# Performance work log

Measured on AMD Instinct MI355X. Metric: run time of the kernel, lower is better.

## Reference

```python
import jax, jax.numpy as jnp
import numpy as np

H = 2048
I = 8192
E = 8
EI = I // E  # expert_intermediate_size = 1024


def setup_inputs() -> dict:
    key = jax.random.key(0)
    k1, k2, k3 = jax.random.split(key, 3)
    B, N = 4, 4096
    x = jax.random.normal(k1, (B, N, H), dtype=jnp.float32)
    position_ids = jnp.arange(B * N, dtype=jnp.int64).reshape(B, N)
    gate_up_proj = 0.02 * jax.random.normal(k2, (E, H, EI * 2), dtype=jnp.float32)
    down_proj = 0.02 * jax.random.normal(k3, (E, EI, H), dtype=jnp.float32)
    return {"x": x, "position_ids": position_ids,
            "gate_up_proj": gate_up_proj, "down_proj": down_proj}


def reference(x, position_ids, gate_up_proj, down_proj):
    # x: [B,N,H]; position_ids: [B,N] (or [N]); expert = pos % E.
    B, N, Hdim = x.shape
    if position_ids.ndim == 1:
        position_ids = jnp.broadcast_to(position_ids[None, :], (B, N))
    eids = (position_ids % E).reshape(B * N)
    flat = x.reshape(B * N, Hdim)

    # Modulo routing is perfectly balanced (N % E == 0 with sequential ids),
    # so group tokens by expert (stable sort) and run dense per-expert GEMMs
    # instead of per-token gathered-weight bmm (same math, no weight blowup).
    T = B * N
    order = jnp.argsort(eids)          # stable in jax -> tokens grouped by expert
    xg = flat[order].reshape(E, T // E, Hdim)            # [E, T/E, H]
    gu = jnp.einsum('ebh,ehk->ebk', xg, gate_up_proj)    # [E, T/E, 2*EI]
    gate, up = gu[..., :EI], gu[..., EI:]
    inter = jax.nn.silu(gate) * up                       # [E, T/E, EI]
    outg = jnp.einsum('ebi,eih->ebh', inter, down_proj)  # [E, T/E, H]
    out = jnp.zeros((T, Hdim), dtype=x.dtype).at[order].set(outg.reshape(T, Hdim))
    return out.reshape(B, N, Hdim)
```

## Files before the change

kernel.cpp:

```cpp
#include <hip/hip_runtime.h>
#include <hip/hip_bf16.h>

typedef unsigned short u16;
typedef __attribute__((ext_vector_type(8))) short short8;
typedef __attribute__((ext_vector_type(8))) unsigned short u16x8;
typedef __attribute__((ext_vector_type(4))) float f32x4;

#define H_DIM 2048
#define EI_DIM 1024
#define NEXP 8

template <int V> struct IC { static constexpr int value = V; };

__device__ __forceinline__ u16 f2bf(float f) {
  __hip_bfloat16 h = __float2bfloat16(f);
  return __builtin_bit_cast(unsigned short, h);
}

__device__ __forceinline__ void load_lds16(const void* g, void* lds) {
  __builtin_amdgcn_global_load_lds(
      (const __attribute__((address_space(1))) unsigned int*)g,
      (__attribute__((address_space(3))) unsigned int*)lds, 16, 0, 0);
}

__global__ __launch_bounds__(1024) void route_kernel(const int* __restrict__ pid,
                                                     int* __restrict__ offcnt,
                                                     int* __restrict__ order, int T) {
  __shared__ int hist[2048];
  __shared__ int lds[256];
  __shared__ int basel[2048];
  int tid = threadIdx.x, w = tid >> 6, lane = tid & 63;
  unsigned long long below = (1ull << lane) - 1ull;
#pragma unroll 1
  for (int i = 0; i < 16; ++i) {
    int seg = w * 16 + i;
    int eid = pid[seg * 64 + lane] & 7;
#pragma unroll
    for (int e = 0; e < NEXP; ++e) {
      unsigned long long m = __ballot(eid == e);
      if (lane == 0) hist[e * 256 + seg] = __popcll(m);
    }
  }
  __syncthreads();
  int v[8], s = 0;
  if (tid < 256) {
#pragma unroll
    for (int j = 0; j < 8; ++j) { v[j] = hist[tid * 8 + j]; s += v[j]; }
    lds[tid] = s;
  }
  __syncthreads();
  for (int d = 1; d < 256; d <<= 1) {
    int t = (tid < 256 && tid >= d) ? lds[tid - d] : 0;
    __syncthreads();
    if (tid < 256) lds[tid] += t;
    __syncthreads();
  }
  if (tid < 256) {
    int run = lds[tid] - s;
#pragma unroll
    for (int j = 0; j < 8; ++j) { basel[tid * 8 + j] = run; run += v[j]; }
  }
  __syncthreads();
  if (tid < NEXP) {
    int o = basel[tid * 256];
    int nx = (tid < NEXP - 1) ? basel[(tid + 1) * 256] : T;
    offcnt[tid] = o;
    offcnt[8 + tid] = nx - o;
  }
#pragma unroll 1
  for (int i = 0; i < 16; ++i) {
    int seg = w * 16 + i;
    int t = seg * 64 + lane;
    int eid = pid[t] & 7;
#pragma unroll
    for (int e = 0; e < NEXP; ++e) {
      unsigned long long m = __ballot(eid == e);
      if (eid == e) order[basel[e * 256 + seg] + __popcll(m & below)] = t;
    }
  }
}

__device__ __forceinline__ void transpose_tile(const float* __restrict__ in,
                                               u16* __restrict__ out, int R, int C, int bx) {
  __shared__ u16 tile[64][65];
  int nbr = R >> 6;
  int per_e = nbr * (C >> 6);
  int e = bx / per_e, rem = bx % per_e;
  int tr = rem % nbr, tc = rem / nbr;
  const float* ine = in + (size_t)e * R * C;
  u16* oute = out + (size_t)e * R * C;
  int r0 = tr * 64, c0 = tc * 64;
  int tid = threadIdx.x;
  int lrow = tid >> 4, lc4 = (tid & 15) * 4;
#pragma unroll
  for (int p = 0; p < 4; ++p) {
    int rl = p * 16 + lrow;
    float4 v = *(const float4*)&ine[(size_t)(r0 + rl) * C + c0 + lc4];
    tile[rl][lc4 + 0] = f2bf(v.x);
    tile[rl][lc4 + 1] = f2bf(v.y);
    tile[rl][lc4 + 2] = f2bf(v.z);
    tile[rl][lc4 + 3] = f2bf(v.w);
  }
  __syncthreads();
#pragma unroll
  for (int p = 0; p < 2; ++p) {
    int idx = p * 256 + tid;
    int jr = idx >> 3, hg = (idx & 7) * 8;
    u16x8 v;
#pragma unroll
    for (int i = 0; i < 8; ++i) v[i] = tile[hg + i][jr];
    *(u16x8*)&oute[(size_t)(c0 + jr) * R + r0 + hg] = v;
  }
}

__global__ __launch_bounds__(256) void convert_kernel(
    const float* __restrict__ gup, const float* __restrict__ dwn, const float* __restrict__ x,
    const int* __restrict__ order, u16* __restrict__ wguT, u16* __restrict__ wdT,
    u16* __restrict__ xg) {
  int bx = blockIdx.x;
  if (bx < 8192) {
    transpose_tile(gup, wguT, 2048, 2048, bx);
  } else if (bx < 8192 + 4096) {
    transpose_tile(dwn, wdT, 1024, 2048, bx - 8192);
  } else {
    int g0 = (bx - 12288) * 8;
    int c = threadIdx.x * 8;
#pragma unroll 1
    for (int r = 0; r < 8; ++r) {
      int g = g0 + r;
      int t = order[g];
      const float* src = x + (size_t)t * H_DIM;
      u16* dst = xg + (size_t)g * H_DIM;
      float4 a = *(const float4*)&src[c];
      float4 b = *(const float4*)&src[c + 4];
      u16x8 vv;
      vv[0] = f2bf(a.x); vv[1] = f2bf(a.y); vv[2] = f2bf(a.z); vv[3] = f2bf(a.w);
      vv[4] = f2bf(b.x); vv[5] = f2bf(b.y); vv[6] = f2bf(b.z); vv[7] = f2bf(b.w);
      *(u16x8*)&dst[c] = vv;
    }
  }
}

template <int KTOT, int KIND>
__device__ __forceinline__ void gemm8_body(
    const u16* __restrict__ A, const u16* __restrict__ Bmat, void* __restrict__ outp,
    const int* __restrict__ offcnt, const int* __restrict__ order, int T) {
  constexpr int NK = KTOT / 64;
  constexpr int ASTR = (KIND == 0) ? H_DIM : EI_DIM;
  constexpr int BSTR = ASTR;
  constexpr size_t BEXP = (size_t)2048 * BSTR;
  __shared__ u16 As[2][2][8192];
  __shared__ u16 Bs[2][2][8192];

  int nwg = gridDim.x;
  int bid = blockIdx.x;
  int bx = (bid & 7) * (nwg >> 3) + (bid >> 3);
  int e = bx >> 6;
  int s = bx & 63;
  int off = offcnt[e], cnt = offcnt[8 + e];
  const u16* Be = Bmat + (size_t)e * BEXP;

  int tid = threadIdx.x, w = tid >> 6, l = tid & 63;
  int wm = w >> 2, wn = w & 3, lr = l & 15, lg = l >> 4;
  int cidx = (lg ^ ((lr >> 1) & 3)) * 8;
  int aRow0 = wm * 128 + lr;
  int bRow0 = wn * 64 + lr;
  int sr[2], sc[2];
#pragma unroll
  for (int j = 0; j < 2; ++j) {
    sr[j] = j * 128 + (tid >> 2);
    int c = tid & 3;
    sc[j] = (c ^ ((sr[j] >> 1) & 3)) * 8;
  }

#pragma unroll 1
  for (int it = s; it < 512; it += 64) {
    int mt = it >> 3, nt = it & 7;
    if (mt * 256 >= cnt) continue;

    const u16* aSrc[2];
    const u16* bSrc[2];
#pragma unroll
    for (int j = 0; j < 2; ++j) {
      int r = sr[j];
      int grow = min(off + mt * 256 + r, T - 1);
      aSrc[j] = A + (size_t)grow * ASTR + sc[j];
      int n;
      if (KIND == 0) {
        int q = r >> 4, rr = r & 15;
        n = ((q & 2) ? EI_DIM : 0) + nt * 128 + ((q >> 2) << 5) + ((q & 1) << 4) + rr;
      } else {
        n = nt * 256 + r;
      }
      bSrc[j] = Be + (size_t)n * BSTR + sc[j];
    }

    auto stageA = [&](int kt, int kh, int buf) {
#pragma unroll
      for (int j = 0; j < 2; ++j)
        load_lds16(aSrc[j] + kt * 64 + kh * 32, &As[buf][kh][j * 4096 + w * 512]);
    };
    auto stageB = [&](int kt, int kh, int buf) {
#pragma unroll
      for (int j = 0; j < 2; ++j)
        load_lds16(bSrc[j] + kt * 64 + kh * 32, &Bs[buf][kh][j * 4096 + w * 512]);
    };

    short8 avA[4], avB[4], bvA[4], bvB[4];
    auto RDA = [&](short8(&dst)[4], int buf, int kh, int h) {
#pragma unroll
      for (int mm = 0; mm < 4; ++mm)
        dst[mm] = *(const short8*)&As[buf][kh][(aRow0 + (h * 4 + mm) * 16) * 32 + cidx];
    };
    auto RDB = [&](short8(&dst)[4], int buf, int kh) {
#pragma unroll
      for (int nn = 0; nn < 4; ++nn)
        dst[nn] = *(const short8*)&Bs[buf][kh][(bRow0 + nn * 16) * 32 + cidx];
    };

    f32x4 acc[8][4];
#pragma unroll
    for (int m = 0; m < 8; ++m)
#pragma unroll
      for (int nn = 0; nn < 4; ++nn) acc[m][nn] = {0.f, 0.f, 0.f, 0.f};

    auto MF = [&](short8(&a)[4], short8(&b)[4], auto HC) {
      constexpr int h = decltype(HC)::value;
      __builtin_amdgcn_s_setprio(1);
#pragma unroll
      for (int mm = 0; mm < 4; ++mm)
#pragma unroll
        for (int nn = 0; nn < 4; ++nn)
          acc[h * 4 + mm][nn] =
              __builtin_amdgcn_mfma_f32_16x16x32_bf16(a[mm], b[nn], acc[h * 4 + mm][nn], 0, 0, 0);
      __builtin_amdgcn_s_setprio(0);
    };

    __syncthreads();

    stageA(0, 0, 0); stageB(0, 0, 0); stageA(0, 1, 0); stageB(0, 1, 0);
    stageB(1, 0, 1); stageA(1, 0, 1); stageB(1, 1, 1);
    asm volatile("s_waitcnt vmcnt(6)" ::: "memory");
    __builtin_amdgcn_s_barrier();
    __builtin_amdgcn_sched_barrier(0);

    auto TILE = [&](int t, auto BC) {
      constexpr int b = decltype(BC)::value;
      constexpr int bn = b ^ 1;
      RDA(avA, b, 0, 0);
      RDB(bvA, b, 0);
      stageA(t + 1, 1, bn);
      MF(avA, bvA, IC<0>{});
      RDA(avB, b, 0, 1);
      __builtin_amdgcn_s_barrier();
      stageB(t + 2, 0, b);
      MF(avB, bvA, IC<1>{});
      RDA(avA, b, 1, 0);
      RDB(bvB, b, 1);
      __builtin_amdgcn_s_barrier();
      stageA(t + 2, 0, b);
      MF(avA, bvB, IC<0>{});
      asm volatile("s_waitcnt vmcnt(4)" ::: "memory");
      RDA(avB, b, 1, 1);
      __builtin_amdgcn_s_barrier();
      stageB(t + 2, 1, b);
      MF(avB, bvB, IC<1>{});
      __builtin_amdgcn_s_barrier();
    };

#pragma unroll 1
    for (int t = 0; t < NK - 3; t += 2) {
      TILE(t, IC<0>{});
      TILE(t + 1, IC<1>{});
    }

    {
      RDA(avA, 0, 0, 0);
      RDB(bvA, 0, 0);
      stageA(NK - 1, 1, 1);
      MF(avA, bvA, IC<0>{});
      RDA(avB, 0, 0, 1);
      __builtin_amdgcn_s_barrier();
      MF(avB, bvA, IC<1>{});
      RDA(avA, 0, 1, 0);
      RDB(bvB, 0, 1);
      __builtin_amdgcn_s_barrier();
      MF(avA, bvB, IC<0>{});
      asm volatile("s_waitcnt vmcnt(0)" ::: "memory");
      RDA(avB, 0, 1, 1);
      __builtin_amdgcn_s_barrier();
      MF(avB, bvB, IC<1>{});
      __builtin_amdgcn_s_barrier();
      RDA(avA, 1, 0, 0);
      RDB(bvA, 1, 0);
      MF(avA, bvA, IC<0>{});
      RDA(avB, 1, 0, 1);
      MF(avB, bvA, IC<1>{});
      RDA(avA, 1, 1, 0);
      RDB(bvB, 1, 1);
      MF(avA, bvB, IC<0>{});
      RDA(avB, 1, 1, 1);
      MF(avB, bvB, IC<1>{});
    }

    if (KIND == 0) {
      u16* inter = (u16*)outp;
#pragma unroll
      for (int m = 0; m < 8; ++m)
#pragma unroll
        for (int nn = 0; nn < 2; ++nn) {
          f32x4 g = acc[m][nn], u = acc[m][nn + 2];
          int icol = nt * 128 + wn * 32 + nn * 16 + lr;
#pragma unroll
          for (int j = 0; j < 4; ++j) {
            int r = wm * 128 + m * 16 + lg * 4 + j;
            int grow = mt * 256 + r;
            if (grow < cnt) {
              float gv = g[j];
              float val = (gv / (1.f + __expf(-gv))) * u[j];
              inter[(size_t)(off + grow) * EI_DIM + icol] = f2bf(val);
            }
          }
        }
    } else {
      float* out = (float*)outp;
#pragma unroll
      for (int m = 0; m < 8; ++m)
#pragma unroll
        for (int j = 0; j < 4; ++j) {
          int r = wm * 128 + m * 16 + lg * 4 + j;
          int grow = mt * 256 + r;
          if (grow < cnt) {
            float* orow = out + (size_t)order[off + grow] * H_DIM + nt * 256 + wn * 64 + lr;
#pragma unroll
            for (int nn = 0; nn < 4; ++nn) orow[nn * 16] = acc[m][nn][j];
          }
        }
    }
  }
}

__global__ __launch_bounds__(512, 2) void gemm_gu_kernel(
    const u16* __restrict__ A, const u16* __restrict__ Bmat, void* __restrict__ outp,
    const int* __restrict__ offcnt, int T) {
  gemm8_body<2048, 0>(A, Bmat, outp, offcnt, nullptr, T);
}

__global__ __launch_bounds__(512, 2) void gemm_down_kernel(
    const u16* __restrict__ A, const u16* __restrict__ Bmat, void* __restrict__ outp,
    const int* __restrict__ offcnt, const int* __restrict__ order, int T) {
  gemm8_body<1024, 1>(A, Bmat, outp, offcnt, order, T);
}

extern "C" void kernel_launch(void* const* d_in, const int* in_sizes, int n_in,
                              void* d_out, int out_size, void* d_ws, size_t ws_size,
                              hipStream_t stream) {
  const float* x = (const float*)d_in[0];
  const int* pid = (const int*)d_in[1];
  const float* gup = (const float*)d_in[2];
  const float* dwn = (const float*)d_in[3];
  float* out = (float*)d_out;

  const int T = in_sizes[1];

  char* ws = (char*)d_ws;
  size_t o = 0;
  auto take = [&](size_t b) { size_t r = o; o += (b + 255) & ~(size_t)255; return r; };
  int* offcnt = (int*)(ws + take(32 * 4));
  int* order = (int*)(ws + take((size_t)T * 4));
  u16* xg = (u16*)(ws + take((size_t)T * H_DIM * 2));
  u16* wguT = (u16*)(ws + take((size_t)NEXP * 2048 * 2048 * 2));
  u16* wdT = (u16*)(ws + take((size_t)NEXP * 2048 * 1024 * 2));
  u16* inter = (u16*)(ws + take((size_t)T * EI_DIM * 2));

  route_kernel<<<1, 1024, 0, stream>>>(pid, offcnt, order, T);
  convert_kernel<<<8192 + 4096 + 2048, 256, 0, stream>>>(gup, dwn, x, order, wguT, wdT, xg);
  gemm_gu_kernel<<<512, 512, 0, stream>>>(xg, wguT, inter, offcnt, T);
  gemm_down_kernel<<<512, 512, 0, stream>>>(inter, wdT, out, offcnt, order, T);
}
```

Before: 338.4 us.

## Restructure GEMM main loop into 8-wave ping-pong schedule with 64-wide K tiles

Reorganizes the LDS layout so each buffer holds a full 64-wide K slice per row with an 8-way XOR swizzle, instead of two 32-wide halves. The main loop becomes a pair-of-tiles schedule of four MFMA bursts per tile, separated by barriers, with global-to-LDS staging interleaved between bursts. The aim is to overlap memory staging with MFMA work and cut LDS bank conflicts. It adds many more barriers and explicit lgkmcnt waits, which could serialize the waves.

```diff
diff --git a/kernel.cpp b/kernel.cpp
--- a/kernel.cpp
+++ b/kernel.cpp
@@ -146,6 +146,7 @@
     const u16* __restrict__ A, const u16* __restrict__ Bmat, void* __restrict__ outp,
     const int* __restrict__ offcnt, const int* __restrict__ order, int T) {
   constexpr int NK = KTOT / 64;
+  constexpr int NPAIR = NK / 2;
   constexpr int ASTR = (KIND == 0) ? H_DIM : EI_DIM;
   constexpr int BSTR = ASTR;
   constexpr size_t BEXP = (size_t)2048 * BSTR;
@@ -156,66 +157,75 @@
   int bid = blockIdx.x;
   int bx = (bid & 7) * (nwg >> 3) + (bid >> 3);
   int e = bx >> 6;
-  int s = bx & 63;
+  int s0 = bx & 63;
   int off = offcnt[e], cnt = offcnt[8 + e];
   const u16* Be = Bmat + (size_t)e * BEXP;
 
   int tid = threadIdx.x, w = tid >> 6, l = tid & 63;
   int wm = w >> 2, wn = w & 3, lr = l & 15, lg = l >> 4;
-  int cidx = (lg ^ ((lr >> 1) & 3)) * 8;
-  int aRow0 = wm * 128 + lr;
-  int bRow0 = wn * 64 + lr;
-  int sr[2], sc[2];
-#pragma unroll
-  for (int j = 0; j < 2; ++j) {
-    sr[j] = j * 128 + (tid >> 2);
-    int c = tid & 3;
-    sc[j] = (c ^ ((sr[j] >> 1) & 3)) * 8;
-  }
-
-#pragma unroll 1
-  for (int it = s; it < 512; it += 64) {
+  int cks[2];
+  cks[0] = ((lg) ^ (lr & 7)) * 8;
+  cks[1] = ((4 + lg) ^ (lr & 7)) * 8;
+  int srow = w * 8 + (l >> 3);
+  int scol = ((l & 7) ^ (l >> 3)) * 8;
+
+#pragma unroll 1
+  for (int it = s0; it < 512; it += 64) {
     int mt = it >> 3, nt = it & 7;
     if (mt * 256 >= cnt) continue;
 
-    const u16* aSrc[2];
-    const u16* bSrc[2];
-#pragma unroll
-    for (int j = 0; j < 2; ++j) {
-      int r = sr[j];
-      int grow = min(off + mt * 256 + r, T - 1);
-      aSrc[j] = A + (size_t)grow * ASTR + sc[j];
-      int n;
-      if (KIND == 0) {
-        int q = r >> 4, rr = r & 15;
-        n = ((q & 2) ? EI_DIM : 0) + nt * 128 + ((q >> 2) << 5) + ((q & 1) << 4) + rr;
-      } else {
-        n = nt * 256 + r;
+    const u16* aS[2][2];
+    const u16* bS[2][2];
+#pragma unroll
+    for (int h = 0; h < 2; ++h)
+#pragma unroll
+      for (int si = 0; si < 2; ++si) {
+        int r = h * 128 + si * 64 + srow;
+        int grow = min(off + mt * 256 + r, T - 1);
+        aS[h][si] = A + (size_t)grow * ASTR + scol;
+        int n;
+        if (KIND == 0) {
+          int q = r >> 4, rr = r & 15;
+          n = ((q & 2) ? EI_DIM : 0) + nt * 128 + ((q >> 2) << 5) + ((q & 1) << 4) + rr;
+        } else {
+          n = nt * 256 + r;
+        }
+        bS[h][si] = Be + (size_t)n * BSTR + scol;
       }
-      bSrc[j] = Be + (size_t)n * BSTR + sc[j];
-    }
-
-    auto stageA = [&](int kt, int kh, int buf) {
-#pragma unroll
-      for (int j = 0; j < 2; ++j)
-        load_lds16(aSrc[j] + kt * 64 + kh * 32, &As[buf][kh][j * 4096 + w * 512]);
-    };
-    auto stageB = [&](int kt, int kh, int buf) {
-#pragma unroll
-      for (int j = 0; j < 2; ++j)
-        load_lds16(bSrc[j] + kt * 64 + kh * 32, &Bs[buf][kh][j * 4096 + w * 512]);
-    };
-
-    short8 avA[4], avB[4], bvA[4], bvB[4];
-    auto RDA = [&](short8(&dst)[4], int buf, int kh, int h) {
+
+    auto stA = [&](int kt, int buf) {
+#pragma unroll
+      for (int h = 0; h < 2; ++h)
+#pragma unroll
+        for (int si = 0; si < 2; ++si)
+          load_lds16(aS[h][si] + kt * 64, &As[buf][h][si * 4096 + w * 512]);
+    };
+    auto stB = [&](int kt, int buf) {
+#pragma unroll
+      for (int h = 0; h < 2; ++h)
+#pragma unroll
+        for (int si = 0; si < 2; ++si)
+          load_lds16(bS[h][si] + kt * 64, &Bs[buf][h][si * 4096 + w * 512]);
+    };
+
+    short8 av[4][2], bv[4][2];
+    auto RDAV = [&](auto BUF, auto MQ) {
+      constexpr int buf = decltype(BUF)::value, mq = decltype(MQ)::value;
 #pragma unroll
       for (int mm = 0; mm < 4; ++mm)
-        dst[mm] = *(const short8*)&As[buf][kh][(aRow0 + (h * 4 + mm) * 16) * 32 + cidx];
-    };
-    auto RDB = [&](short8(&dst)[4], int buf, int kh) {
+#pragma unroll
+        for (int ks = 0; ks < 2; ++ks)
+          av[mm][ks] =
+              *(const short8*)&As[buf][wm][(mq * 64 + mm * 16 + lr) * 64 + cks[ks]];
+    };
+    auto RDBV = [&](auto BUF) {
+      constexpr int buf = decltype(BUF)::value;
 #pragma unroll
       for (int nn = 0; nn < 4; ++nn)
-        dst[nn] = *(const short8*)&Bs[buf][kh][(bRow0 + nn * 16) * 32 + cidx];
+#pragma unroll
+        for (int ks = 0; ks < 2; ++ks)
+          bv[nn][ks] = *(const short8*)&Bs[buf][wn >> 1]
+                           [((wn & 1) * 64 + nn * 16 + lr) * 64 + cks[ks]];
     };
 
     f32x4 acc[8][4];
@@ -224,84 +234,90 @@
 #pragma unroll
       for (int nn = 0; nn < 4; ++nn) acc[m][nn] = {0.f, 0.f, 0.f, 0.f};
 
-    auto MF = [&](short8(&a)[4], short8(&b)[4], auto HC) {
-      constexpr int h = decltype(HC)::value;
+    auto BURST = [&](auto MQ, auto NQ) {
+      constexpr int mq = decltype(MQ)::value, nq = decltype(NQ)::value;
       __builtin_amdgcn_s_setprio(1);
 #pragma unroll
       for (int mm = 0; mm < 4; ++mm)
 #pragma unroll
-        for (int nn = 0; nn < 4; ++nn)
-          acc[h * 4 + mm][nn] =
-              __builtin_amdgcn_mfma_f32_16x16x32_bf16(a[mm], b[nn], acc[h * 4 + mm][nn], 0, 0, 0);
+        for (int nn = 0; nn < 2; ++nn)
+#pragma unroll
+          for (int ks = 0; ks < 2; ++ks)
+            acc[mq * 4 + mm][nq * 2 + nn] = __builtin_amdgcn_mfma_f32_16x16x32_bf16(
+                av[mm][ks], bv[nq * 2 + nn][ks], acc[mq * 4 + mm][nq * 2 + nn], 0, 0, 0);
       __builtin_amdgcn_s_setprio(0);
     };
 
+#define BAR __builtin_amdgcn_s_barrier()
+#define LGKM0                                          \
+  do {                                                 \
+    asm volatile("s_waitcnt lgkmcnt(0)" ::: "memory"); \
+    __builtin_amdgcn_sched_barrier(0);                 \
+  } while (0)
+
     __syncthreads();
 
-    stageA(0, 0, 0); stageB(0, 0, 0); stageA(0, 1, 0); stageB(0, 1, 0);
-    stageB(1, 0, 1); stageA(1, 0, 1); stageB(1, 1, 1);
-    asm volatile("s_waitcnt vmcnt(6)" ::: "memory");
-    __builtin_amdgcn_s_barrier();
+    stA(0, 0);
+    stB(0, 0);
+    stB(1, 1);
+    stA(1, 1);
+    asm volatile("s_waitcnt vmcnt(8)" ::: "memory");
+    BAR;
     __builtin_amdgcn_sched_barrier(0);
 
-    auto TILE = [&](int t, auto BC) {
-      constexpr int b = decltype(BC)::value;
-      constexpr int bn = b ^ 1;
-      RDA(avA, b, 0, 0);
-      RDB(bvA, b, 0);
-      stageA(t + 1, 1, bn);
-      MF(avA, bvA, IC<0>{});
-      RDA(avB, b, 0, 1);
-      __builtin_amdgcn_s_barrier();
-      stageB(t + 2, 0, b);
-      MF(avB, bvA, IC<1>{});
-      RDA(avA, b, 1, 0);
-      RDB(bvB, b, 1);
-      __builtin_amdgcn_s_barrier();
-      stageA(t + 2, 0, b);
-      MF(avA, bvB, IC<0>{});
-      asm volatile("s_waitcnt vmcnt(4)" ::: "memory");
-      RDA(avB, b, 1, 1);
-      __builtin_amdgcn_s_barrier();
-      stageB(t + 2, 1, b);
-      MF(avB, bvB, IC<1>{});
-      __builtin_amdgcn_s_barrier();
-    };
-
-#pragma unroll 1
-    for (int t = 0; t < NK - 3; t += 2) {
-      TILE(t, IC<0>{});
-      TILE(t + 1, IC<1>{});
-    }
-
-    {
-      RDA(avA, 0, 0, 0);
-      RDB(bvA, 0, 0);
-      stageA(NK - 1, 1, 1);
-      MF(avA, bvA, IC<0>{});
-      RDA(avB, 0, 0, 1);
-      __builtin_amdgcn_s_barrier();
-      MF(avB, bvA, IC<1>{});
-      RDA(avA, 0, 1, 0);
-      RDB(bvB, 0, 1);
-      __builtin_amdgcn_s_barrier();
-      MF(avA, bvB, IC<0>{});
-      asm volatile("s_waitcnt vmcnt(0)" ::: "memory");
-      RDA(avB, 0, 1, 1);
-      __builtin_amdgcn_s_barrier();
-      MF(avB, bvB, IC<1>{});
-      __builtin_amdgcn_s_barrier();
-      RDA(avA, 1, 0, 0);
-      RDB(bvA, 1, 0);
-      MF(avA, bvA, IC<0>{});
-      RDA(avB, 1, 0, 1);
-      MF(avB, bvA, IC<1>{});
-      RDA(avA, 1, 1, 0);
-      RDB(bvB, 1, 1);
-      MF(avA, bvB, IC<0>{});
-      RDA(avB, 1, 1, 1);
-      MF(avB, bvB, IC<1>{});
-    }
+    auto PAIR = [&](int t2, int t3, auto LASTC) {
+      constexpr bool last = decltype(LASTC)::value;
+      RDAV(IC<0>{}, IC<0>{});
+      RDBV(IC<0>{});
+      BAR;
+      LGKM0;
+      BURST(IC<0>{}, IC<0>{});
+      BAR;
+      if constexpr (!last) stB(t2, 0);
+      BAR;
+      BURST(IC<0>{}, IC<1>{});
+      BAR;
+      RDAV(IC<0>{}, IC<1>{});
+      BAR;
+      LGKM0;
+      BURST(IC<1>{}, IC<0>{});
+      BAR;
+      if constexpr (!last) stA(t2, 0);
+      BAR;
+      BURST(IC<1>{}, IC<1>{});
+      if constexpr (!last)
+        asm volatile("s_waitcnt vmcnt(8)" ::: "memory");
+      else
+        asm volatile("s_waitcnt vmcnt(0)" ::: "memory");
+      BAR;
+      RDAV(IC<1>{}, IC<0>{});
+      RDBV(IC<1>{});
+      BAR;
+      LGKM0;
+      BURST(IC<0>{}, IC<0>{});
+      BAR;
+      if constexpr (!last) stB(t3, 1);
+      BAR;
+      BURST(IC<0>{}, IC<1>{});
+      BAR;
+      RDAV(IC<1>{}, IC<1>{});
+      BAR;
+      LGKM0;
+      BURST(IC<1>{}, IC<0>{});
+      BAR;
+      if constexpr (!last) stA(t3, 1);
+      BAR;
+      BURST(IC<1>{}, IC<1>{});
+      if constexpr (!last) asm volatile("s_waitcnt vmcnt(8)" ::: "memory");
+      BAR;
+    };
+
+#pragma unroll 1
+    for (int i = 0; i < NPAIR - 1; ++i) PAIR(2 * i + 2, 2 * i + 3, IC<0>{});
+    PAIR(0, 0, IC<1>{});
+
+#undef BAR
+#undef LGKM0
 
     if (KIND == 0) {
       u16* inter = (u16*)outp;
```

Result: slower. 356.2 us (+5.3%).
